# Kernel optimization log

Measured on AMD Instinct MI355X. Metric: run time of the kernel, lower is better.

## Reference

```python
import jax, jax.numpy as jnp
import numpy as np

B, C, RXD, E, P, OSIZE = 64, 4, 64, 512, 4, 256


def setup_inputs() -> dict:
    key = jax.random.key(0)
    ks = jax.random.split(key, 6)
    x = jax.random.normal(ks[0], (B, C, RXD, E), dtype=jnp.float32)
    # rxd permutation (gather form of the one-hot permuteRxdMatrix matmul)
    rxd_perm = jax.random.permutation(ks[1], RXD)
    # E permutation and its compositions: permuter = permuter @ permuteEMatrix
    # in column-index form: idx_{p+1}[j] = idx_p[e_perm[j]]
    e_perm = np.array(jax.random.permutation(ks[2], E))
    idx = e_perm.copy()
    cols = []
    for _ in range(P):
        cols.append(idx.copy())
        idx = idx[e_perm]
    e_idx = jnp.asarray(np.stack(cols, axis=1))  # (E, P) int
    # sign selected at the single nonzero entry of each permutation column
    signs = (jax.random.uniform(ks[3], (E, P)) > 0.5).astype(jnp.float32) * 2.0 - 1.0
    fan_in = RXD * E * P
    W = jax.random.normal(ks[4], (OSIZE, fan_in), dtype=jnp.float32) / np.float32(np.sqrt(fan_in))
    b = jax.random.normal(ks[5], (OSIZE,), dtype=jnp.float32) * 0.01
    return {"x": x, "rxd_perm": rxd_perm, "e_idx": e_idx, "signs": signs, "W": W, "b": b}


def reference(x, rxd_perm, e_idx, signs, W, b):
    Bb, Cc, R, Ee = x.shape
    Pp = e_idx.shape[1]
    # permute rxd axis (exact equivalent of x.transpose @ one-hot matrix)
    out = x[:, :, rxd_perm, :]                      # (B,C,R,E)
    # signed E-permutations for all P powers (exact equiv of dense matmul
    # with permuteETensor * signTensor, which has one signed nonzero per column)
    out = out[..., e_idx] * signs                   # (B,C,R,E,P)
    L = R * Ee
    pieces = []
    for p in range(Pp):
        k = 2 ** p
        v = out[..., p].reshape(Bb, Cc, L)
        if k == 1:
            pieces.append(v)                        # pool+unpool with k=1 is identity
        else:
            Lp = ((L + k - 1) // k) * k             # ceil_mode padding
            vp = jnp.pad(v, ((0, 0), (0, 0), (0, Lp - L)), constant_values=-jnp.inf)
            w = vp.reshape(Bb, Cc, Lp // k, k)
            am = jnp.argmax(w, axis=-1)             # first max, matching torch MaxPool1d
            mx = jnp.max(w, axis=-1)
            onehot = jnp.arange(k) == am[..., None]
            # MaxUnpool: max value at argmax position, zeros elsewhere
            pieces.append(jnp.where(onehot, mx[..., None], 0.0).reshape(Bb, Cc, Lp))
    pieces[-1] = pieces[-1][:, :, :L]               # truncate last piece to L
    cat = jnp.concatenate(pieces, axis=2)           # (B,C,L*P) since L % k == 0
    return cat @ W.T + b                            # (B,C,OSIZE)
```

## Files before the change

kernel.cpp:

```cpp
#include <hip/hip_runtime.h>
#include <stdint.h>

#define B_ 64
#define C_ 4
#define R_ 64
#define E_ 512
#define P_ 4
#define OS_ 256
#define L_ (R_*E_)
#define K_ (L_*P_)
#define M_ (B_*C_)

#define BM 256
#define BN 128
#define BK 32
#define Z_ 256
#define KCH (K_/Z_)
#define ITERS (KCH/BK)

typedef float  floatx4 __attribute__((ext_vector_type(4)));
typedef short  shortx8 __attribute__((ext_vector_type(8)));

#define GLDS16(g, l) __builtin_amdgcn_global_load_lds(                      \
    (const __attribute__((address_space(1))) void*)(g),                     \
    (__attribute__((address_space(3))) void*)(l), 16, 0, 0)

static __device__ __forceinline__ unsigned short f2bf(float f) {
  union { float f; unsigned int u; } v; v.f = f;
  unsigned int u = v.u;
  u += 0x7fffu + ((u >> 16) & 1u);
  return (unsigned short)(u >> 16);
}

__global__ __launch_bounds__(512) void build_A(
    const float* __restrict__ x, const int* __restrict__ rxd_perm,
    const int* __restrict__ e_idx, const float* __restrict__ signs,
    unsigned short* __restrict__ A) {
  const int blk = blockIdx.x;
  const int bc  = blk >> 3;
  const int rg  = blk & 7;
  const int t   = threadIdx.x;
  __shared__ float xr[8][E_];

  #pragma unroll
  for (int i = 0; i < 2; ++i) {
    const int q   = i * 512 + t;
    const int row = q >> 7;
    const int c4  = q & 127;
    const float4 v = *(const float4*)(
        x + ((size_t)(bc * R_ + rxd_perm[rg * 8 + row])) * E_ + c4 * 4);
    *(float4*)(&xr[row][c4 * 4]) = v;
  }
  __syncthreads();

  const int rloc = t >> 6;
  const int e0   = (t & 63) * 8;
  const int r    = rg * 8 + rloc;
  const float* xp = xr[rloc];

  float v[4][8];
  #pragma unroll
  for (int i = 0; i < 8; ++i) {
    const uint4  ei = *(const uint4*)(e_idx + (size_t)(e0 + i) * 4);
    const float4 sg = *(const float4*)(signs + (size_t)(e0 + i) * 4);
    v[0][i] = xp[ei.x] * sg.x;
    v[1][i] = xp[ei.y] * sg.y;
    v[2][i] = xp[ei.z] * sg.z;
    v[3][i] = xp[ei.w] * sg.w;
  }

  unsigned short* dst = A + (size_t)bc * K_ + (size_t)r * E_ + e0;
  shortx8 o;

  #pragma unroll
  for (int i = 0; i < 8; ++i) o[i] = (short)f2bf(v[0][i]);
  *(shortx8*)(dst) = o;

  #pragma unroll
  for (int j = 0; j < 4; ++j) {
    const float a = v[1][2 * j], b = v[1][2 * j + 1];
    const bool first = (a >= b);
    o[2 * j]     = (short)f2bf(first ? a : 0.0f);
    o[2 * j + 1] = (short)f2bf(first ? 0.0f : b);
  }
  *(shortx8*)(dst + L_) = o;

  #pragma unroll
  for (int j = 0; j < 2; ++j) {
    int am = 0; float m = v[2][4 * j];
    #pragma unroll
    for (int i = 1; i < 4; ++i)
      if (v[2][4 * j + i] > m) { m = v[2][4 * j + i]; am = i; }
    #pragma unroll
    for (int i = 0; i < 4; ++i) o[4 * j + i] = (short)f2bf(i == am ? m : 0.0f);
  }
  *(shortx8*)(dst + 2 * L_) = o;

  {
    int am = 0; float m = v[3][0];
    #pragma unroll
    for (int i = 1; i < 8; ++i)
      if (v[3][i] > m) { m = v[3][i]; am = i; }
    #pragma unroll
    for (int i = 0; i < 8; ++i) o[i] = (short)f2bf(i == am ? m : 0.0f);
  }
  *(shortx8*)(dst + 3 * L_) = o;
}

__global__ __launch_bounds__(512, 4) void gemm_splitk(
    const unsigned short* __restrict__ A, const float* __restrict__ W,
    float* __restrict__ Pp) {
  __shared__ unsigned short As[2][BM * BK];
  __shared__ unsigned short Ws[2][BN * BK];
  const int t    = threadIdx.x;
  const int lane = t & 63;
  const int wv   = t >> 6;

  const int id = blockIdx.x;
  const int ny = (id >> 3) & 1;
  const int z  = (id & 7) | ((id >> 4) << 3);
  const int nBase = ny * BN;
  const size_t k0base = (size_t)z * KCH;

  const int wm   = (wv >> 1) * 64;
  const int wn   = (wv & 1) * 64;
  const int lrow = lane & 15;
  const int quad = lane >> 4;
  const int rx   = lrow & 3;
  const int aCh  = (lane & 3) ^ ((lane >> 2) & 3);

  const int wrow = t >> 2;
  const int wch  = t & 3;
  const float* wbase = W + (size_t)(nBase + wrow) * K_ + wch * 8;
  const int wslot = (wrow * 4 + (wch ^ (wrow & 3))) * 8;

  floatx4 acc[4][4];
  #pragma unroll
  for (int i = 0; i < 4; ++i)
    #pragma unroll
    for (int j = 0; j < 4; ++j) acc[i][j] = {0.f, 0.f, 0.f, 0.f};

  float4 wr0, wr1;

  auto loadW = [&](size_t k0) {
    wr0 = *(const float4*)(wbase + k0);
    wr1 = *(const float4*)(wbase + k0 + 4);
  };
  auto stageA = [&](int buf, size_t k0) {
    #pragma unroll
    for (int c = 0; c < 2; ++c) {
      const int sblk = (wv * 2 + c) * 64;
      const int row  = (sblk >> 2) + (lane >> 2);
      GLDS16(A + (size_t)row * K_ + k0 + (size_t)aCh * 8, &As[buf][sblk * 8]);
    }
  };
  auto writeW = [&](int buf) {
    shortx8 b0;
    b0[0] = (short)f2bf(wr0.x); b0[1] = (short)f2bf(wr0.y);
    b0[2] = (short)f2bf(wr0.z); b0[3] = (short)f2bf(wr0.w);
    b0[4] = (short)f2bf(wr1.x); b0[5] = (short)f2bf(wr1.y);
    b0[6] = (short)f2bf(wr1.z); b0[7] = (short)f2bf(wr1.w);
    *(shortx8*)(&Ws[buf][wslot]) = b0;
  };
  auto compute = [&](int buf) {
    const int ch = quad;
    shortx8 af[4], wf[4];
    #pragma unroll
    for (int ti = 0; ti < 4; ++ti) {
      const int row = wm + ti * 16 + lrow;
      af[ti] = *(const shortx8*)(&As[buf][(row * 4 + (ch ^ rx)) * 8]);
    }
    #pragma unroll
    for (int tj = 0; tj < 4; ++tj) {
      const int row = wn + tj * 16 + lrow;
      wf[tj] = *(const shortx8*)(&Ws[buf][(row * 4 + (ch ^ rx)) * 8]);
    }
    #pragma unroll
    for (int ti = 0; ti < 4; ++ti)
      #pragma unroll
      for (int tj = 0; tj < 4; ++tj)
        acc[ti][tj] = __builtin_amdgcn_mfma_f32_16x16x32_bf16(
            af[ti], wf[tj], acc[ti][tj], 0, 0, 0);
  };

  loadW(k0base);
  stageA(0, k0base);
  writeW(0);
  __syncthreads();

  for (int it = 0; it < ITERS; ++it) {
    const int b = it & 1;
    const bool pf = (it + 1 < ITERS);
    if (pf) {
      const size_t k0n = k0base + (size_t)(it + 1) * BK;
      loadW(k0n);
      stageA(b ^ 1, k0n);
    }
    compute(b);
    if (pf) writeW(b ^ 1);
    __syncthreads();
  }

  float* Pz = Pp + (size_t)z * (M_ * OS_);
  #pragma unroll
  for (int ti = 0; ti < 4; ++ti)
    #pragma unroll
    for (int tj = 0; tj < 4; ++tj)
      #pragma unroll
      for (int j = 0; j < 4; ++j) {
        const int m = wm + ti * 16 + quad * 4 + j;
        const int n = nBase + wn + tj * 16 + lrow;
        Pz[(size_t)m * OS_ + n] = acc[ti][tj][j];
      }
}

__global__ __launch_bounds__(64) void reduce_out(
    const float* __restrict__ Pp, const float* __restrict__ bias,
    float* __restrict__ out) {
  const int i4 = blockIdx.x * 64 + threadIdx.x;
  const float* p = Pp + (size_t)i4 * 4;
  float4 s = {0.f, 0.f, 0.f, 0.f};
  #pragma unroll 8
  for (int zz = 0; zz < Z_; ++zz) {
    const float4 v = *(const float4*)(p + (size_t)zz * (M_ * OS_));
    s.x += v.x; s.y += v.y; s.z += v.z; s.w += v.w;
  }
  const float4 bb = *(const float4*)(bias + ((i4 * 4) & (OS_ - 1)));
  float4 o = {s.x + bb.x, s.y + bb.y, s.z + bb.z, s.w + bb.w};
  *(float4*)(out + (size_t)i4 * 4) = o;
}

extern "C" void kernel_launch(void* const* d_in, const int* in_sizes, int n_in,
                              void* d_out, int out_size, void* d_ws, size_t ws_size,
                              hipStream_t stream) {
  const float* x        = (const float*)d_in[0];
  const int*   rxd_perm = (const int*)d_in[1];
  const int*   e_idx    = (const int*)d_in[2];
  const float* signs    = (const float*)d_in[3];
  const float* W        = (const float*)d_in[4];
  const float* bias     = (const float*)d_in[5];
  float* out = (float*)d_out;

  unsigned short* A = (unsigned short*)d_ws;
  float* Pp = (float*)((char*)d_ws + (size_t)M_ * K_ * 2);

  build_A<<<dim3(M_ * 8), dim3(512), 0, stream>>>(x, rxd_perm, e_idx, signs, A);
  gemm_splitk<<<dim3(2 * Z_), dim3(512), 0, stream>>>(A, W, Pp);
  reduce_out<<<dim3((M_ * OS_ / 4) / 64), dim3(64), 0, stream>>>(Pp, bias, out);
}
```

Baseline: 282.8 us.

## Pre-convert W to bf16 and retile A/W into k8-major layouts for direct LDS loads

Adds a prep kernel that builds A and also converts W to bf16 in one launch. Both are written in a k8-chunk-major, row-minor layout, so the GEMM can stage both operands with global_load_lds and needs no register round-trip, conversion or swizzle. The reduce kernel now splits the z-sum across two thread halves with an LDS combine. This adds a full write and re-read of a bf16 W copy in every call, in exchange for halving W bytes read by the GEMM and simplifying its inner loop.

```diff
diff --git a/kernel.cpp b/kernel.cpp
--- a/kernel.cpp
+++ b/kernel.cpp
@@ -8,8 +8,10 @@
 #define P_ 4
 #define OS_ 256
 #define L_ (R_*E_)
-#define K_ (L_*P_)
-#define M_ (B_*C_)
+#define K_ (L_*E8_DUMMY)
+#undef K_
+#define K_ 131072
+#define M_ 256
 
 #define BM 256
 #define BN 128
@@ -32,86 +34,125 @@
   return (unsigned short)(u >> 16);
 }
 
-__global__ __launch_bounds__(512) void build_A(
+__global__ __launch_bounds__(512) void prep(
     const float* __restrict__ x, const int* __restrict__ rxd_perm,
     const int* __restrict__ e_idx, const float* __restrict__ signs,
-    unsigned short* __restrict__ A) {
-  const int blk = blockIdx.x;
-  const int bc  = blk >> 3;
-  const int rg  = blk & 7;
-  const int t   = threadIdx.x;
-  __shared__ float xr[8][E_];
-
-  #pragma unroll
-  for (int i = 0; i < 2; ++i) {
-    const int q   = i * 512 + t;
-    const int row = q >> 7;
-    const int c4  = q & 127;
-    const float4 v = *(const float4*)(
-        x + ((size_t)(bc * R_ + rxd_perm[rg * 8 + row])) * E_ + c4 * 4);
-    *(float4*)(&xr[row][c4 * 4]) = v;
-  }
-  __syncthreads();
-
-  const int rloc = t >> 6;
-  const int e0   = (t & 63) * 8;
-  const int r    = rg * 8 + rloc;
-  const float* xp = xr[rloc];
-
-  float v[4][8];
-  #pragma unroll
-  for (int i = 0; i < 8; ++i) {
-    const uint4  ei = *(const uint4*)(e_idx + (size_t)(e0 + i) * 4);
-    const float4 sg = *(const float4*)(signs + (size_t)(e0 + i) * 4);
-    v[0][i] = xp[ei.x] * sg.x;
-    v[1][i] = xp[ei.y] * sg.y;
-    v[2][i] = xp[ei.z] * sg.z;
-    v[3][i] = xp[ei.w] * sg.w;
-  }
-
-  unsigned short* dst = A + (size_t)bc * K_ + (size_t)r * E_ + e0;
-  shortx8 o;
-
-  #pragma unroll
-  for (int i = 0; i < 8; ++i) o[i] = (short)f2bf(v[0][i]);
-  *(shortx8*)(dst) = o;
-
-  #pragma unroll
-  for (int j = 0; j < 4; ++j) {
-    const float a = v[1][2 * j], b = v[1][2 * j + 1];
-    const bool first = (a >= b);
-    o[2 * j]     = (short)f2bf(first ? a : 0.0f);
-    o[2 * j + 1] = (short)f2bf(first ? 0.0f : b);
-  }
-  *(shortx8*)(dst + L_) = o;
-
-  #pragma unroll
-  for (int j = 0; j < 2; ++j) {
-    int am = 0; float m = v[2][4 * j];
-    #pragma unroll
-    for (int i = 1; i < 4; ++i)
-      if (v[2][4 * j + i] > m) { m = v[2][4 * j + i]; am = i; }
-    #pragma unroll
-    for (int i = 0; i < 4; ++i) o[4 * j + i] = (short)f2bf(i == am ? m : 0.0f);
-  }
-  *(shortx8*)(dst + 2 * L_) = o;
-
-  {
-    int am = 0; float m = v[3][0];
-    #pragma unroll
-    for (int i = 1; i < 8; ++i)
-      if (v[3][i] > m) { m = v[3][i]; am = i; }
-    #pragma unroll
-    for (int i = 0; i < 8; ++i) o[i] = (short)f2bf(i == am ? m : 0.0f);
-  }
-  *(shortx8*)(dst + 3 * L_) = o;
+    const float* __restrict__ W,
+    unsigned short* __restrict__ A2, unsigned short* __restrict__ W2) {
+  __shared__ __align__(16) unsigned char smem[64 * 33 * 16];
+  const int t = threadIdx.x;
+
+  if (blockIdx.x < 2048) {
+    const int blk = blockIdx.x;
+    const int bcg = blk >> 6;
+    const int r   = blk & 63;
+    float (*xr)[E_] = (float(*)[E_])smem;
+    const int pr = rxd_perm[r];
+
+    #pragma unroll
+    for (int i = 0; i < 2; ++i) {
+      const int q   = i * 512 + t;
+      const int row = q >> 7;
+      const int c4  = q & 127;
+      const int bc  = bcg * 8 + row;
+      *(float4*)(&xr[row][c4 * 4]) =
+          *(const float4*)(x + ((size_t)bc * R_ + pr) * E_ + c4 * 4);
+    }
+    __syncthreads();
+
+    const int bcLoc = t >> 6;
+    const int lane  = t & 63;
+    const int e0    = lane * 8;
+    const int bc    = bcg * 8 + bcLoc;
+    const float* xp = xr[bcLoc];
+
+    float v[4][8];
+    #pragma unroll
+    for (int i = 0; i < 8; ++i) {
+      const uint4  ei = *(const uint4*)(e_idx + (size_t)(e0 + i) * 4);
+      const float4 sg = *(const float4*)(signs + (size_t)(e0 + i) * 4);
+      v[0][i] = xp[ei.x] * sg.x;
+      v[1][i] = xp[ei.y] * sg.y;
+      v[2][i] = xp[ei.z] * sg.z;
+      v[3][i] = xp[ei.w] * sg.w;
+    }
+
+    const size_t gbase = (size_t)(r * 64 + lane) * 256 + bc;
+    shortx8 o;
+
+    #pragma unroll
+    for (int i = 0; i < 8; ++i) o[i] = (short)f2bf(v[0][i]);
+    *(shortx8*)(A2 + gbase * 8) = o;
+
+    #pragma unroll
+    for (int j = 0; j < 4; ++j) {
+      const float a = v[1][2 * j], b = v[1][2 * j + 1];
+      const bool first = (a >= b);
+      o[2 * j]     = (short)f2bf(first ? a : 0.0f);
+      o[2 * j + 1] = (short)f2bf(first ? 0.0f : b);
+    }
+    *(shortx8*)(A2 + (gbase + (size_t)4096 * 256) * 8) = o;
+
+    #pragma unroll
+    for (int j = 0; j < 2; ++j) {
+      int am = 0; float m = v[2][4 * j];
+      #pragma unroll
+      for (int i = 1; i < 4; ++i)
+        if (v[2][4 * j + i] > m) { m = v[2][4 * j + i]; am = i; }
+      #pragma unroll
+      for (int i = 0; i < 4; ++i) o[4 * j + i] = (short)f2bf(i == am ? m : 0.0f);
+    }
+    *(shortx8*)(A2 + (gbase + (size_t)2 * 4096 * 256) * 8) = o;
+
+    {
+      int am = 0; float m = v[3][0];
+      #pragma unroll
+      for (int i = 1; i < 8; ++i)
+        if (v[3][i] > m) { m = v[3][i]; am = i; }
+      #pragma unroll
+      for (int i = 0; i < 8; ++i) o[i] = (short)f2bf(i == am ? m : 0.0f);
+    }
+    *(shortx8*)(A2 + (gbase + (size_t)3 * 4096 * 256) * 8) = o;
+
+  } else {
+    const int cb = blockIdx.x - 2048;
+    const int nb = cb & 7;
+    const int kb = cb >> 3;
+    const int nbase  = nb * 32;
+    const int k8base = kb * 64;
+    unsigned short* T = (unsigned short*)smem;
+
+    const int nloc = t >> 4, seg = t & 15;
+    const float* wp = W + (size_t)(nbase + nloc) * K_ + (size_t)kb * 512 + seg * 32;
+    #pragma unroll
+    for (int j = 0; j < 4; ++j) {
+      const float4 a0 = *(const float4*)(wp + j * 8);
+      const float4 a1 = *(const float4*)(wp + j * 8 + 4);
+      shortx8 g;
+      g[0] = (short)f2bf(a0.x); g[1] = (short)f2bf(a0.y);
+      g[2] = (short)f2bf(a0.z); g[3] = (short)f2bf(a0.w);
+      g[4] = (short)f2bf(a1.x); g[5] = (short)f2bf(a1.y);
+      g[6] = (short)f2bf(a1.z); g[7] = (short)f2bf(a1.w);
+      const int k8loc = seg * 4 + j;
+      *(shortx8*)(&T[(k8loc * 33 + nloc) * 8]) = g;
+    }
+    __syncthreads();
+
+    const int k8loc = t >> 3, part = t & 7;
+    unsigned short* wdst = W2 + ((size_t)(k8base + k8loc) * 256 + nbase) * 8;
+    #pragma unroll
+    for (int j = 0; j < 4; ++j) {
+      const int g = j * 8 + part;
+      *(shortx8*)(wdst + (size_t)g * 8) = *(const shortx8*)(&T[(k8loc * 33 + g) * 8]);
+    }
+  }
 }
 
 __global__ __launch_bounds__(512, 4) void gemm_splitk(
-    const unsigned short* __restrict__ A, const float* __restrict__ W,
+    const unsigned short* __restrict__ A2, const unsigned short* __restrict__ W2,
     float* __restrict__ Pp) {
-  __shared__ unsigned short As[2][BM * BK];
-  __shared__ unsigned short Ws[2][BN * BK];
+  __shared__ unsigned short As[2][4 * 256 * 8];
+  __shared__ unsigned short Ws[2][4 * 128 * 8];
   const int t    = threadIdx.x;
   const int lane = t & 63;
   const int wv   = t >> 6;
@@ -120,19 +161,11 @@
   const int ny = (id >> 3) & 1;
   const int z  = (id & 7) | ((id >> 4) << 3);
   const int nBase = ny * BN;
-  const size_t k0base = (size_t)z * KCH;
 
   const int wm   = (wv >> 1) * 64;
   const int wn   = (wv & 1) * 64;
   const int lrow = lane & 15;
   const int quad = lane >> 4;
-  const int rx   = lrow & 3;
-  const int aCh  = (lane & 3) ^ ((lane >> 2) & 3);
-
-  const int wrow = t >> 2;
-  const int wch  = t & 3;
-  const float* wbase = W + (size_t)(nBase + wrow) * K_ + wch * 8;
-  const int wslot = (wrow * 4 + (wch ^ (wrow & 3))) * 8;
 
   floatx4 acc[4][4];
   #pragma unroll
@@ -140,41 +173,26 @@
     #pragma unroll
     for (int j = 0; j < 4; ++j) acc[i][j] = {0.f, 0.f, 0.f, 0.f};
 
-  float4 wr0, wr1;
-
-  auto loadW = [&](size_t k0) {
-    wr0 = *(const float4*)(wbase + k0);
-    wr1 = *(const float4*)(wbase + k0 + 4);
-  };
-  auto stageA = [&](int buf, size_t k0) {
+  auto stage = [&](int buf, int it) {
+    const size_t g0 = (size_t)(z * 64 + it * 4) * 256;
     #pragma unroll
     for (int c = 0; c < 2; ++c) {
-      const int sblk = (wv * 2 + c) * 64;
-      const int row  = (sblk >> 2) + (lane >> 2);
-      GLDS16(A + (size_t)row * K_ + k0 + (size_t)aCh * 8, &As[buf][sblk * 8]);
-    }
-  };
-  auto writeW = [&](int buf) {
-    shortx8 b0;
-    b0[0] = (short)f2bf(wr0.x); b0[1] = (short)f2bf(wr0.y);
-    b0[2] = (short)f2bf(wr0.z); b0[3] = (short)f2bf(wr0.w);
-    b0[4] = (short)f2bf(wr1.x); b0[5] = (short)f2bf(wr1.y);
-    b0[6] = (short)f2bf(wr1.z); b0[7] = (short)f2bf(wr1.w);
-    *(shortx8*)(&Ws[buf][wslot]) = b0;
+      const int slot = (wv * 2 + c) * 64 + lane;
+      GLDS16(A2 + (g0 + slot) * 8, &As[buf][slot * 8]);
+    }
+    const int wslot = wv * 64 + lane;
+    const int slab  = wslot >> 7;
+    const int nloc  = wslot & 127;
+    GLDS16(W2 + (g0 + (size_t)slab * 256 + nBase + nloc) * 8, &Ws[buf][wslot * 8]);
   };
   auto compute = [&](int buf) {
-    const int ch = quad;
     shortx8 af[4], wf[4];
     #pragma unroll
-    for (int ti = 0; ti < 4; ++ti) {
-      const int row = wm + ti * 16 + lrow;
-      af[ti] = *(const shortx8*)(&As[buf][(row * 4 + (ch ^ rx)) * 8]);
-    }
-    #pragma unroll
-    for (int tj = 0; tj < 4; ++tj) {
-      const int row = wn + tj * 16 + lrow;
-      wf[tj] = *(const shortx8*)(&Ws[buf][(row * 4 + (ch ^ rx)) * 8]);
-    }
+    for (int ti = 0; ti < 4; ++ti)
+      af[ti] = *(const shortx8*)(&As[buf][(quad * 256 + wm + ti * 16 + lrow) * 8]);
+    #pragma unroll
+    for (int tj = 0; tj < 4; ++tj)
+      wf[tj] = *(const shortx8*)(&Ws[buf][(quad * 128 + wn + tj * 16 + lrow) * 8]);
     #pragma unroll
     for (int ti = 0; ti < 4; ++ti)
       #pragma unroll
@@ -183,21 +201,13 @@
             af[ti], wf[tj], acc[ti][tj], 0, 0, 0);
   };
 
-  loadW(k0base);
-  stageA(0, k0base);
-  writeW(0);
+  stage(0, 0);
   __syncthreads();
 
   for (int it = 0; it < ITERS; ++it) {
     const int b = it & 1;
-    const bool pf = (it + 1 < ITERS);
-    if (pf) {
-      const size_t k0n = k0base + (size_t)(it + 1) * BK;
-      loadW(k0n);
-      stageA(b ^ 1, k0n);
-    }
+    if (it + 1 < ITERS) stage(b ^ 1, it + 1);
     compute(b);
-    if (pf) writeW(b ^ 1);
     __syncthreads();
   }
 
@@ -214,20 +224,29 @@
       }
 }
 
-__global__ __launch_bounds__(64) void reduce_out(
+__global__ __launch_bounds__(256) void reduce_out(
     const float* __restrict__ Pp, const float* __restrict__ bias,
     float* __restrict__ out) {
-  const int i4 = blockIdx.x * 64 + threadIdx.x;
-  const float* p = Pp + (size_t)i4 * 4;
+  __shared__ float4 part[128];
+  const int t    = threadIdx.x;
+  const int i4   = blockIdx.x * 128 + (t & 127);
+  const int half = t >> 7;
+  const float* p = Pp + (size_t)i4 * 4 + (size_t)half * 128 * (M_ * OS_);
   float4 s = {0.f, 0.f, 0.f, 0.f};
   #pragma unroll 8
-  for (int zz = 0; zz < Z_; ++zz) {
+  for (int zz = 0; zz < 128; ++zz) {
     const float4 v = *(const float4*)(p + (size_t)zz * (M_ * OS_));
     s.x += v.x; s.y += v.y; s.z += v.z; s.w += v.w;
   }
-  const float4 bb = *(const float4*)(bias + ((i4 * 4) & (OS_ - 1)));
-  float4 o = {s.x + bb.x, s.y + bb.y, s.z + bb.z, s.w + bb.w};
-  *(float4*)(out + (size_t)i4 * 4) = o;
+  if (half) part[t & 127] = s;
+  __syncthreads();
+  if (!half) {
+    const float4 q = part[t];
+    const float4 bb = *(const float4*)(bias + ((i4 * 4) & (OS_ - 1)));
+    float4 o = {s.x + q.x + bb.x, s.y + q.y + bb.y,
+                s.z + q.z + bb.z, s.w + q.w + bb.w};
+    *(float4*)(out + (size_t)i4 * 4) = o;
+  }
 }
 
 extern "C" void kernel_launch(void* const* d_in, const int* in_sizes, int n_in,
@@ -241,10 +260,11 @@
   const float* bias     = (const float*)d_in[5];
   float* out = (float*)d_out;
 
-  unsigned short* A = (unsigned short*)d_ws;
-  float* Pp = (float*)((char*)d_ws + (size_t)M_ * K_ * 2);
-
-  build_A<<<dim3(M_ * 8), dim3(512), 0, stream>>>(x, rxd_perm, e_idx, signs, A);
-  gemm_splitk<<<dim3(2 * Z_), dim3(512), 0, stream>>>(A, W, Pp);
-  reduce_out<<<dim3((M_ * OS_ / 4) / 64), dim3(64), 0, stream>>>(Pp, bias, out);
-}
+  unsigned short* A2 = (unsigned short*)d_ws;
+  unsigned short* W2 = (unsigned short*)((char*)d_ws + 67108864);
+  float*          Pp = (float*)((char*)d_ws + 134217728);
+
+  prep<<<dim3(4096), dim3(512), 0, stream>>>(x, rxd_perm, e_idx, signs, W, A2, W2);
+  gemm_splitk<<<dim3(2 * Z_), dim3(512), 0, stream>>>(A2, W2, Pp);
+  reduce_out<<<dim3(128), dim3(256), 0, stream>>>(Pp, bias, out);
+}
```

Result: slower. 335.0 us (+18.5%).
